# Performance work log

Hardware: AMD Instinct MI355X
Metric: run time of the kernel (lower is better)

The kernel has to match this reference:

```python
import jax, jax.numpy as jnp
import numpy as np

N_QUBITS = 10
DIM = 768
N_LAYERS = 3
BATCH = 2048


def setup_inputs() -> dict:
    key = jax.random.key(0)
    ks = jax.random.split(key, 5)
    z_i = jax.random.normal(ks[0], (BATCH, DIM), jnp.float32)
    W_in = jax.random.normal(ks[1], (DIM, N_QUBITS), jnp.float32) / np.sqrt(DIM).astype(np.float32)
    b_in = jnp.zeros((N_QUBITS,), jnp.float32)
    # torch.rand(shape) * pi  -> uniform [0, pi)
    weights = jax.random.uniform(ks[2], (N_LAYERS, N_QUBITS, 3), jnp.float32) * np.float32(np.pi)
    W_out = jax.random.normal(ks[3], (N_QUBITS, DIM), jnp.float32) / np.sqrt(N_QUBITS).astype(np.float32)
    b_out = jnp.zeros((DIM,), jnp.float32)
    return {"z_i": z_i, "W_in": W_in, "b_in": b_in, "weights": weights, "W_out": W_out, "b_out": b_out}


def _apply_gate(state, gate, q):
    """Apply a 1-qubit gate on wire q (wire 0 = most significant bit, PennyLane order).
    state: (B, 2**n) complex64; gate: (2,2) shared or (B,2,2) per-sample."""
    B, dim = state.shape
    left = 2 ** q
    right = dim // (2 * left)
    s = state.reshape(B, left, 2, right)
    eq = 'bij,bkjl->bkil' if gate.ndim == 3 else 'ij,bkjl->bkil'
    return jnp.einsum(eq, gate, s).reshape(B, dim)


def _apply_cnot(state, c, t, n):
    B = state.shape[0]
    s = state.reshape((B,) + (2,) * n)
    s = jnp.moveaxis(s, (1 + c, 1 + t), (1, 2))
    # control=1 block: flip target bit
    s = jnp.concatenate([s[:, :1], s[:, 1:, ::-1]], axis=1)
    s = jnp.moveaxis(s, (1, 2), (1 + c, 1 + t))
    return s.reshape(B, -1)


def _circuit(angles, weights):
    """AngleEmbedding (RX) + StronglyEntanglingLayers (Rot + ring of CNOTs), PauliZ expvals."""
    B, n = angles.shape
    L = weights.shape[0]
    state = jnp.zeros((B, 2 ** n), jnp.complex64).at[:, 0].set(1.0)
    # AngleEmbedding: RX(a) = [[cos(a/2), -i sin(a/2)], [-i sin(a/2), cos(a/2)]], per sample
    half = (0.5 * angles).astype(jnp.complex64)
    c = jnp.cos(half)
    s = -1j * jnp.sin(half)
    for q in range(n):
        g = jnp.stack([jnp.stack([c[:, q], s[:, q]], -1),
                       jnp.stack([s[:, q], c[:, q]], -1)], -2)  # (B,2,2)
        state = _apply_gate(state, g, q)
    wc = weights.astype(jnp.complex64)
    for l in range(L):
        for q in range(n):
            phi, theta, omega = wc[l, q, 0], wc[l, q, 1], wc[l, q, 2]
            ct = jnp.cos(0.5 * theta)
            st = jnp.sin(0.5 * theta)
            # Rot(phi,theta,omega) = RZ(omega) RY(theta) RZ(phi)
            g = jnp.stack([
                jnp.stack([jnp.exp(-0.5j * (phi + omega)) * ct, -jnp.exp(0.5j * (phi - omega)) * st]),
                jnp.stack([jnp.exp(-0.5j * (phi - omega)) * st, jnp.exp(0.5j * (phi + omega)) * ct]),
            ])
            state = _apply_gate(state, g, q)
        r = (l % (n - 1)) + 1  # PennyLane default ranges
        for i in range(n):
            state = _apply_cnot(state, i, (i + r) % n, n)
    probs = (state.real ** 2 + state.imag ** 2).reshape((B,) + (2,) * n)
    evs = []
    for w in range(n):
        axes = tuple(a for a in range(1, n + 1) if a != 1 + w)
        pw = probs.sum(axes)  # (B, 2)
        evs.append(pw[:, 0] - pw[:, 1])  # <Z_w>
    return jnp.stack(evs, -1)  # (B, n) float32


def reference(z_i, W_in, b_in, weights, W_out, b_out):
    # torch code detaches the projected angles before the qnode (.cpu().detach())
    angles = jax.lax.stop_gradient(z_i @ W_in + b_in)  # (B, n_qubits)
    evs = _circuit(angles, weights)
    return evs @ W_out + b_out  # (B, classical_input_dim)
```

## Files before the change

### kernel.cpp

```cpp
#include <hip/hip_runtime.h>

typedef float f2 __attribute__((ext_vector_type(2)));
typedef float f4 __attribute__((ext_vector_type(4)));

constexpr int NQ   = 10;
constexpr int CDIM = 768;
constexpr int NL   = 3;
constexpr int NREG = 16;
constexpr int WPB  = 4;


template<int CTRL>
__device__ __forceinline__ float dppmov(float x) {
    return __int_as_float(__builtin_amdgcn_update_dpp(
        __float_as_int(x), __float_as_int(x), CTRL, 0xF, 0xF, true));
}

template<int MASK>
__device__ __forceinline__ float lxor(float x, int lane) {
    static_assert(MASK == 1 || MASK == 2 || MASK == 4 || MASK == 8, "");
    if constexpr (MASK == 1)      return dppmov<0xB1>(x);
    else if constexpr (MASK == 2) return dppmov<0x4E>(x);
    else if constexpr (MASK == 4) {
        const float a = dppmov<0x104>(x);
        const float b = dppmov<0x114>(x);
        return ((lane >> 2) & 1) ? b : a;
    }
    else                          return dppmov<0x128>(x);
}

template<int B>
__device__ __forceinline__ void swap2(float x, float& lo, float& hi) {
    const unsigned xu = __float_as_uint(x);
#if __has_builtin(__builtin_amdgcn_permlane16_swap) && __has_builtin(__builtin_amdgcn_permlane32_swap)
    if constexpr (B == 4) {
        auto r = __builtin_amdgcn_permlane16_swap(xu, xu, false, false);
        lo = __uint_as_float(r[0]); hi = __uint_as_float(r[1]);
    } else {
        auto r = __builtin_amdgcn_permlane32_swap(xu, xu, false, false);
        lo = __uint_as_float(r[0]); hi = __uint_as_float(r[1]);
    }
#else
    float d, s;
    if constexpr (B == 4)
        asm("v_mov_b32 %0, %2\n\tv_mov_b32 %1, %2\n\ts_nop 1\n\t"
            "v_permlane16_swap_b32 %0, %1"
            : "=&v"(d), "=&v"(s) : "v"(x));
    else
        asm("v_mov_b32 %0, %2\n\tv_mov_b32 %1, %2\n\ts_nop 1\n\t"
            "v_permlane32_swap_b32 %0, %1"
            : "=&v"(d), "=&v"(s) : "v"(x));
    lo = d; hi = s;
#endif
}

__device__ __forceinline__ float wave_sum(float v) {
    v += dppmov<0xB1>(v);
    v += dppmov<0x4E>(v);
    v += dppmov<0x141>(v);
    v += dppmov<0x140>(v);
    float lo, hi;
    swap2<4>(v, lo, hi); v = lo + hi;
    swap2<5>(v, lo, hi); v = lo + hi;
    return v;
}


__device__ __forceinline__ f2 swapneg(f2 b) { f2 r; r.x = -b.y; r.y = b.x; return r; }
__device__ __forceinline__ f2 cmul(f2 a, f2 b) { return b * a.x + swapneg(b) * a.y; }
__device__ __forceinline__ f2 cfma(f2 a, f2 b, f2 acc) { return acc + b * a.x + swapneg(b) * a.y; }


template<int B>
__device__ __forceinline__ void gate_bit(f2 (&v)[NREG], int lane,
                                         f2 g00, f2 g01, f2 g10, f2 g11) {
    if constexpr (B >= 6) {
        constexpr int rb = B - 6;
#pragma unroll
        for (int p = 0; p < NREG / 2; ++p) {
            const int r0 = ((p >> rb) << (rb + 1)) | (p & ((1 << rb) - 1));
            const int r1 = r0 | (1 << rb);
            const f2 a0 = v[r0], a1 = v[r1];
            v[r0] = cfma(g01, a1, cmul(g00, a0));
            v[r1] = cfma(g11, a1, cmul(g10, a0));
        }
    } else if constexpr (B >= 4) {
        const bool hb = (lane >> B) & 1;
        const f2 A  = hb ? g10 : g00;
        const f2 Bc = hb ? g11 : g01;
#pragma unroll
        for (int r = 0; r < NREG; ++r) {
            float lx, hx, ly, hy;
            swap2<B>(v[r].x, lx, hx);
            swap2<B>(v[r].y, ly, hy);
            f2 lo; lo.x = lx; lo.y = ly;
            f2 hi; hi.x = hx; hi.y = hy;
            v[r] = cfma(Bc, hi, cmul(A, lo));
        }
    } else {
        const bool hb = (lane >> B) & 1;
        const f2 cO = hb ? g11 : g00;
        const f2 cP = hb ? g10 : g01;
#pragma unroll
        for (int r = 0; r < NREG; ++r) {
            f2 p;
            p.x = lxor<(1 << B)>(v[r].x, lane);
            p.y = lxor<(1 << B)>(v[r].y, lane);
            v[r] = cfma(cP, p, cmul(cO, v[r]));
        }
    }
}

template<int BT>
__device__ __forceinline__ float partner(float x, int lane) {
    if constexpr (BT >= 4) {
        float lo, hi; swap2<BT>(x, lo, hi);
        return ((lane >> BT) & 1) ? lo : hi;
    } else return lxor<(1 << BT)>(x, lane);
}


template<int BC, int BT>
__device__ __forceinline__ void cnot(f2 (&v)[NREG], int lane) {
    if constexpr (BC >= 6 && BT >= 6) {
        constexpr int rc = BC - 6, rt = BT - 6;
#pragma unroll
        for (int r = 0; r < NREG; ++r)
            if (((r >> rc) & 1) && !((r >> rt) & 1)) {
                const int r1 = r | (1 << rt);
                const f2 t = v[r]; v[r] = v[r1]; v[r1] = t;
            }
    } else if constexpr (BC >= 6) {
        constexpr int rc = BC - 6;
#pragma unroll
        for (int r = 0; r < NREG; ++r)
            if ((r >> rc) & 1) {
                f2 n;
                n.x = partner<BT>(v[r].x, lane);
                n.y = partner<BT>(v[r].y, lane);
                v[r] = n;
            }
    } else if constexpr (BT >= 6) {
        constexpr int rt = BT - 6;
        const bool c = (lane >> BC) & 1;
#pragma unroll
        for (int p = 0; p < NREG / 2; ++p) {
            const int r0 = ((p >> rt) << (rt + 1)) | (p & ((1 << rt) - 1));
            const int r1 = r0 | (1 << rt);
            const f2 a = v[r0], b = v[r1];
            v[r0] = c ? b : a;
            v[r1] = c ? a : b;
        }
    } else {
        const bool c = (lane >> BC) & 1;
#pragma unroll
        for (int r = 0; r < NREG; ++r) {
            f2 n;
            n.x = c ? partner<BT>(v[r].x, lane) : v[r].x;
            n.y = c ? partner<BT>(v[r].y, lane) : v[r].y;
            v[r] = n;
        }
    }
}


template<int Q = 0>
__device__ __forceinline__ void rot_layer_lds(f2 (&v)[NREG], int lane,
                                              const float4* g ) {
    if constexpr (Q < NQ) {
        const float4 p0 = g[Q * 2];
        const float4 p1 = g[Q * 2 + 1];
        f2 g00 = {p0.x, p0.y}, g01 = {p0.z, p0.w};
        f2 g10 = {p1.x, p1.y}, g11 = {p1.z, p1.w};
        gate_bit<9 - Q>(v, lane, g00, g01, g10, g11);
        rot_layer_lds<Q + 1>(v, lane, g);
    }
}

template<int L, int I = 0>
__device__ __forceinline__ void cnot_ring(f2 (&v)[NREG], int lane) {
    if constexpr (I < NQ) {
        constexpr int R = (L % (NQ - 1)) + 1;
        cnot<9 - I, 9 - ((I + R) % NQ)>(v, lane);
        cnot_ring<L, I + 1>(v, lane);
    }
}

constexpr unsigned ring2_mask(int w) {
    unsigned M[NQ] = {};
    for (int i = 0; i < NQ; ++i) M[i] = 1u << (9 - i);
    for (int i = 0; i < NQ; ++i) M[(i + 3) % NQ] ^= M[i];
    return M[w];
}

template<unsigned MR>
__device__ __forceinline__ float regsum16(const float (&pr)[NREG]) {
    float s = 0.f;
#pragma unroll
    for (int r = 0; r < NREG; ++r)
        s = (__builtin_popcount((unsigned)r & MR) & 1) ? s - pr[r] : s + pr[r];
    return s;
}

template<int W = 0>
__device__ __forceinline__ void measure_all(const float (&pr)[NREG], int lane,
                                            float (&ev)[NQ]) {
    if constexpr (W < NQ) {
        constexpr unsigned m  = ring2_mask(W);
        constexpr unsigned mr = (m >> 6) & 0xFu;
        constexpr unsigned ml = m & 63u;
        float s = regsum16<mr>(pr);
        if constexpr (ml != 0) {
            const unsigned flip = (unsigned)((__popc(lane & (int)ml) & 1)) << 31;
            s = __uint_as_float(__float_as_uint(s) ^ flip);
        }
        ev[W] = wave_sum(s);
        measure_all<W + 1>(pr, lane, ev);
    }
}

__global__ __launch_bounds__(64 * WPB, 2) void qembed(
    const float* __restrict__ z,
    const float* __restrict__ Win,
    const float* __restrict__ bin,
    const float* __restrict__ wts,
    const float* __restrict__ Wout,
    const float* __restrict__ bout,
    float* __restrict__ out)
{
    __shared__ float4 gl4[NL][NQ][2];

    const int wave = threadIdx.x >> 6;
    const int lane = threadIdx.x & 63;
    const int samp = blockIdx.x * WPB + wave;

    if (threadIdx.x < NL * NQ) {
        const int li = threadIdx.x / NQ, q = threadIdx.x % NQ;
        const float* wp = wts + (li * NQ + q) * 3;
        const float phi = wp[0], th = wp[1], om = wp[2];
        float st, ct, sA, cA, sB, cB;
        __sincosf(0.5f * th, &st, &ct);
        __sincosf(0.5f * (phi + om), &sA, &cA);
        __sincosf(0.5f * (phi - om), &sB, &cB);
        gl4[li][q][0] = make_float4( ct * cA, -ct * sA, -st * cB, -st * sB);
        gl4[li][q][1] = make_float4( st * cB, -st * sB,  ct * cA,  ct * sA);
    }

    float ang[NQ];
    {
        const float* zrow = z + (size_t)samp * CDIM;
        f2 a5[NQ / 2];
#pragma unroll
        for (int h = 0; h < NQ / 2; ++h) a5[h] = (f2){0.f, 0.f};
#pragma unroll
        for (int j = 0; j < 3; ++j) {
            const int kb = 4 * (lane + 64 * j);
            const float4 zv = *(const float4*)(zrow + kb);
            float w40[40];
#pragma unroll
            for (int t = 0; t < 10; ++t) {
                const float4 u = *(const float4*)(Win + (size_t)kb * NQ + 4 * t);
                w40[4 * t] = u.x; w40[4 * t + 1] = u.y;
                w40[4 * t + 2] = u.z; w40[4 * t + 3] = u.w;
            }
            const float zc[4] = {zv.x, zv.y, zv.z, zv.w};
#pragma unroll
            for (int c = 0; c < 4; ++c)
#pragma unroll
                for (int h = 0; h < NQ / 2; ++h) {
                    f2 w; w.x = w40[c * 10 + 2 * h]; w.y = w40[c * 10 + 2 * h + 1];
                    a5[h] += w * zc[c];
                }
        }
#pragma unroll
        for (int h = 0; h < NQ / 2; ++h) {
            ang[2 * h]     = wave_sum(a5[h].x) + bin[2 * h];
            ang[2 * h + 1] = wave_sum(a5[h].y) + bin[2 * h + 1];
        }
    }

    __syncthreads();

    f2 f0[NQ], f1[NQ];
#pragma unroll
    for (int q = 0; q < NQ; ++q) {
        const float4 p0 = gl4[0][q][0];
        const float4 p1 = gl4[0][q][1];
        float s, c;
        __sincosf(0.5f * ang[q], &s, &c);
        f2 a, b;
        a.x = p0.x * c + s * p0.w;  a.y = p0.y * c - s * p0.z;
        b.x = p1.x * c + s * p1.w;  b.y = p1.y * c - s * p1.z;
        f0[q] = a; f1[q] = b;
    }

    const int gray = lane ^ (lane >> 1);
    const int l0 = lane & 1;
    const int l5 = (lane >> 5) & 1;
    f2 G0 = ((gray >> 0) & 1) ? f1[9] : f0[9];
    f2 G1 = ((gray >> 1) & 1) ? f1[8] : f0[8];
    f2 G2 = ((gray >> 2) & 1) ? f1[7] : f0[7];
    f2 G3 = ((gray >> 3) & 1) ? f1[6] : f0[6];
    f2 G4 = ((gray >> 4) & 1) ? f1[5] : f0[5];
    const f2 L5 = cmul(cmul(G0, G1), cmul(G2, cmul(G3, G4)));
    f2 B5[2];
    B5[0] = l5 ? f1[4] : f0[4];
    B5[1] = l5 ? f0[4] : f1[4];
    f2 D8[2], E9[2];
    D8[0] = l0 ? f1[1] : f0[1];
    D8[1] = l0 ? f0[1] : f1[1];
    E9[0] = l0 ? f1[0] : f0[0];
    E9[1] = l0 ? f0[0] : f1[0];

    f2 P1[2];
    P1[0] = cmul(L5, B5[0]);
    P1[1] = cmul(L5, B5[1]);
    f2 P2[4];
#pragma unroll
    for (int r1b = 0; r1b < 2; ++r1b)
#pragma unroll
        for (int r0b = 0; r0b < 2; ++r0b)
            P2[r0b + 2 * r1b] = cmul(P1[r0b], (r0b ^ r1b) ? f1[3] : f0[3]);
    f2 P3[8];
#pragma unroll
    for (int r2b = 0; r2b < 2; ++r2b)
#pragma unroll
        for (int p = 0; p < 4; ++p)
            P3[p + 4 * r2b] = cmul(P2[p], (((p >> 1) & 1) ^ r2b) ? f1[2] : f0[2]);
    f2 W[4];
#pragma unroll
    for (int d = 0; d < 2; ++d)
#pragma unroll
        for (int u = 0; u < 2; ++u)
            W[u + 2 * d] = cmul(D8[u], E9[d]);

    f2 v[NREG];
#pragma unroll
    for (int r = 0; r < NREG; ++r) {
        const int r2b = (r >> 2) & 1, r3b = (r >> 3) & 1;
        v[r] = cmul(P3[r & 7], W[(r2b ^ r3b) + 2 * r3b]);
    }

#pragma unroll 1
    for (int l = 0; l < 2; ++l) {
        rot_layer_lds(v, lane, &gl4[l + 1][0][0]);
        if (l == 0) cnot_ring<1>(v, lane);
    }

    float pr[NREG];
#pragma unroll
    for (int r = 0; r < NREG; ++r) pr[r] = v[r].x * v[r].x + v[r].y * v[r].y;

    float ev[NQ];
    measure_all(pr, lane, ev);

#pragma unroll 1
    for (int ch = 0; ch < 3; ++ch) {
        const int d0 = ch * 256 + lane * 4;
        f4 w4[NQ];
#pragma unroll
        for (int q = 0; q < NQ; ++q) w4[q] = *(const f4*)(Wout + q * CDIM + d0);
        f4 o = *(const f4*)(bout + d0);
#pragma unroll
        for (int q = 0; q < NQ; ++q) o += w4[q] * ev[q];
        *(f4*)(out + (size_t)samp * CDIM + d0) = o;
    }
}

extern "C" void kernel_launch(void* const* d_in, const int* in_sizes, int n_in,
                              void* d_out, int out_size, void* d_ws, size_t ws_size,
                              hipStream_t stream) {
    const float* z    = (const float*)d_in[0];
    const float* Win  = (const float*)d_in[1];
    const float* bin  = (const float*)d_in[2];
    const float* wts  = (const float*)d_in[3];
    const float* Wout = (const float*)d_in[4];
    const float* bout = (const float*)d_in[5];
    float* outp       = (float*)d_out;

    const int batch  = in_sizes[0] / CDIM;
    const int blocks = batch / WPB;
    qembed<<<blocks, 64 * WPB, 0, stream>>>(z, Win, bin, wts, Wout, bout, outp);
}
```

Measured before the change: 27.18 us.

## Split each sample's statevector across two waves with LDS exchange for top qubit

Each sample now gets two wavefronts: each holds half the 1024-amplitude state (8 registers instead of 16), with the most significant qubit encoded by wave index. Gates and CNOTs that touch that qubit swap data through shared memory with block barriers, and expectation values are combined across the two waves through LDS. The output projection is also split between the waves. This halves the per-thread register footprint and doubles the wave count, which should raise occupancy and latency hiding. The cost is extra LDS traffic and several __syncthreads per layer.

After: 30.07 us. 1.11x slower.

```diff
diff --git a/kernel.cpp b/kernel.cpp
--- a/kernel.cpp
+++ b/kernel.cpp
@@ -1,13 +1,11 @@
 #include <hip/hip_runtime.h>
 
 typedef float f2 __attribute__((ext_vector_type(2)));
-typedef float f4 __attribute__((ext_vector_type(4)));
 
 constexpr int NQ   = 10;
 constexpr int CDIM = 768;
 constexpr int NL   = 3;
-constexpr int NREG = 16;
-constexpr int WPB  = 4;
+constexpr int NR   = 8;
 
 
 template<int CTRL>
@@ -44,12 +42,10 @@
     float d, s;
     if constexpr (B == 4)
         asm("v_mov_b32 %0, %2\n\tv_mov_b32 %1, %2\n\ts_nop 1\n\t"
-            "v_permlane16_swap_b32 %0, %1"
-            : "=&v"(d), "=&v"(s) : "v"(x));
+            "v_permlane16_swap_b32 %0, %1" : "=&v"(d), "=&v"(s) : "v"(x));
     else
         asm("v_mov_b32 %0, %2\n\tv_mov_b32 %1, %2\n\ts_nop 1\n\t"
-            "v_permlane32_swap_b32 %0, %1"
-            : "=&v"(d), "=&v"(s) : "v"(x));
+            "v_permlane32_swap_b32 %0, %1" : "=&v"(d), "=&v"(s) : "v"(x));
     lo = d; hi = s;
 #endif
 }
@@ -72,12 +68,13 @@
 
 
 template<int B>
-__device__ __forceinline__ void gate_bit(f2 (&v)[NREG], int lane,
+__device__ __forceinline__ void gate_bit(f2 (&v)[NR], int lane,
                                          f2 g00, f2 g01, f2 g10, f2 g11) {
+    static_assert(B <= 8, "");
     if constexpr (B >= 6) {
         constexpr int rb = B - 6;
 #pragma unroll
-        for (int p = 0; p < NREG / 2; ++p) {
+        for (int p = 0; p < NR / 2; ++p) {
             const int r0 = ((p >> rb) << (rb + 1)) | (p & ((1 << rb) - 1));
             const int r1 = r0 | (1 << rb);
             const f2 a0 = v[r0], a1 = v[r1];
@@ -89,7 +86,7 @@
         const f2 A  = hb ? g10 : g00;
         const f2 Bc = hb ? g11 : g01;
 #pragma unroll
-        for (int r = 0; r < NREG; ++r) {
+        for (int r = 0; r < NR; ++r) {
             float lx, hx, ly, hy;
             swap2<B>(v[r].x, lx, hx);
             swap2<B>(v[r].y, ly, hy);
@@ -102,7 +99,7 @@
         const f2 cO = hb ? g11 : g00;
         const f2 cP = hb ? g10 : g01;
 #pragma unroll
-        for (int r = 0; r < NREG; ++r) {
+        for (int r = 0; r < NR; ++r) {
             f2 p;
             p.x = lxor<(1 << B)>(v[r].x, lane);
             p.y = lxor<(1 << B)>(v[r].y, lane);
@@ -121,11 +118,44 @@
 
 
 template<int BC, int BT>
-__device__ __forceinline__ void cnot(f2 (&v)[NREG], int lane) {
-    if constexpr (BC >= 6 && BT >= 6) {
+__device__ __forceinline__ void cnot(f2 (&v)[NR], int lane, int hs,
+                                     f2* mybuf, const f2* pbuf) {
+    if constexpr (BC == 9) {
+        if (hs) {
+            if constexpr (BT >= 6) {
+                constexpr int rt = BT - 6;
+#pragma unroll
+                for (int p = 0; p < NR / 2; ++p) {
+                    const int r0 = ((p >> rt) << (rt + 1)) | (p & ((1 << rt) - 1));
+                    const int r1 = r0 | (1 << rt);
+                    const f2 t = v[r0]; v[r0] = v[r1]; v[r1] = t;
+                }
+            } else {
+#pragma unroll
+                for (int r = 0; r < NR; ++r) {
+                    f2 n;
+                    n.x = partner<BT>(v[r].x, lane);
+                    n.y = partner<BT>(v[r].y, lane);
+                    v[r] = n;
+                }
+            }
+        }
+    } else if constexpr (BT == 9) {
+        static_assert(BC < 6, "");
+#pragma unroll
+        for (int r = 0; r < NR; ++r) mybuf[r * 64 + lane] = v[r];
+        __syncthreads();
+        const bool c = (lane >> BC) & 1;
+#pragma unroll
+        for (int r = 0; r < NR; ++r) {
+            const f2 pv = pbuf[r * 64 + lane];
+            v[r] = c ? pv : v[r];
+        }
+        __syncthreads();
+    } else if constexpr (BC >= 6 && BT >= 6) {
         constexpr int rc = BC - 6, rt = BT - 6;
 #pragma unroll
-        for (int r = 0; r < NREG; ++r)
+        for (int r = 0; r < NR; ++r)
             if (((r >> rc) & 1) && !((r >> rt) & 1)) {
                 const int r1 = r | (1 << rt);
                 const f2 t = v[r]; v[r] = v[r1]; v[r1] = t;
@@ -133,7 +163,7 @@
     } else if constexpr (BC >= 6) {
         constexpr int rc = BC - 6;
 #pragma unroll
-        for (int r = 0; r < NREG; ++r)
+        for (int r = 0; r < NR; ++r)
             if ((r >> rc) & 1) {
                 f2 n;
                 n.x = partner<BT>(v[r].x, lane);
@@ -144,7 +174,7 @@
         constexpr int rt = BT - 6;
         const bool c = (lane >> BC) & 1;
 #pragma unroll
-        for (int p = 0; p < NREG / 2; ++p) {
+        for (int p = 0; p < NR / 2; ++p) {
             const int r0 = ((p >> rt) << (rt + 1)) | (p & ((1 << rt) - 1));
             const int r1 = r0 | (1 << rt);
             const f2 a = v[r0], b = v[r1];
@@ -154,7 +184,7 @@
     } else {
         const bool c = (lane >> BC) & 1;
 #pragma unroll
-        for (int r = 0; r < NREG; ++r) {
+        for (int r = 0; r < NR; ++r) {
             f2 n;
             n.x = c ? partner<BT>(v[r].x, lane) : v[r].x;
             n.y = c ? partner<BT>(v[r].y, lane) : v[r].y;
@@ -164,25 +194,45 @@
 }
 
 
-template<int Q = 0>
-__device__ __forceinline__ void rot_layer_lds(f2 (&v)[NREG], int lane,
-                                              const float4* g ) {
+__device__ __forceinline__ void rot_wave_gate(f2 (&v)[NR], int lane, int hs,
+                                              f2* mybuf, const f2* pbuf,
+                                              const float4* g) {
+    const float4 p0 = g[0];
+    const float4 p1 = g[1];
+    f2 g00 = {p0.x, p0.y}, g01 = {p0.z, p0.w};
+    f2 g10 = {p1.x, p1.y}, g11 = {p1.z, p1.w};
+    const f2 cO = hs ? g11 : g00;
+    const f2 cP = hs ? g10 : g01;
+#pragma unroll
+    for (int r = 0; r < NR; ++r) mybuf[r * 64 + lane] = v[r];
+    __syncthreads();
+#pragma unroll
+    for (int r = 0; r < NR; ++r) {
+        const f2 pv = pbuf[r * 64 + lane];
+        v[r] = cfma(cP, pv, cmul(cO, v[r]));
+    }
+    __syncthreads();
+}
+
+template<int Q = 1>
+__device__ __forceinline__ void rot_layer_rest(f2 (&v)[NR], int lane,
+                                               const float4* g ) {
     if constexpr (Q < NQ) {
         const float4 p0 = g[Q * 2];
         const float4 p1 = g[Q * 2 + 1];
         f2 g00 = {p0.x, p0.y}, g01 = {p0.z, p0.w};
         f2 g10 = {p1.x, p1.y}, g11 = {p1.z, p1.w};
         gate_bit<9 - Q>(v, lane, g00, g01, g10, g11);
-        rot_layer_lds<Q + 1>(v, lane, g);
-    }
-}
-
-template<int L, int I = 0>
-__device__ __forceinline__ void cnot_ring(f2 (&v)[NREG], int lane) {
+        rot_layer_rest<Q + 1>(v, lane, g);
+    }
+}
+
+template<int I = 0>
+__device__ __forceinline__ void cnot_ring1(f2 (&v)[NR], int lane, int hs,
+                                           f2* mybuf, const f2* pbuf) {
     if constexpr (I < NQ) {
-        constexpr int R = (L % (NQ - 1)) + 1;
-        cnot<9 - I, 9 - ((I + R) % NQ)>(v, lane);
-        cnot_ring<L, I + 1>(v, lane);
+        cnot<9 - I, 9 - ((I + 2) % NQ)>(v, lane, hs, mybuf, pbuf);
+        cnot_ring1<I + 1>(v, lane, hs, mybuf, pbuf);
     }
 }
 
@@ -194,32 +244,35 @@
 }
 
 template<unsigned MR>
-__device__ __forceinline__ float regsum16(const float (&pr)[NREG]) {
+__device__ __forceinline__ float regsum8(const float (&pr)[NR]) {
     float s = 0.f;
 #pragma unroll
-    for (int r = 0; r < NREG; ++r)
+    for (int r = 0; r < NR; ++r)
         s = (__builtin_popcount((unsigned)r & MR) & 1) ? s - pr[r] : s + pr[r];
     return s;
 }
 
 template<int W = 0>
-__device__ __forceinline__ void measure_all(const float (&pr)[NREG], int lane,
+__device__ __forceinline__ void measure_all(const float (&pr)[NR], int lane, int hs,
                                             float (&ev)[NQ]) {
     if constexpr (W < NQ) {
         constexpr unsigned m  = ring2_mask(W);
-        constexpr unsigned mr = (m >> 6) & 0xFu;
+        constexpr unsigned mr = (m >> 6) & 0x7u;
+        constexpr unsigned mw = (m >> 9) & 0x1u;
         constexpr unsigned ml = m & 63u;
-        float s = regsum16<mr>(pr);
-        if constexpr (ml != 0) {
-            const unsigned flip = (unsigned)((__popc(lane & (int)ml) & 1)) << 31;
-            s = __uint_as_float(__float_as_uint(s) ^ flip);
-        }
+        float s = regsum8<mr>(pr);
+        unsigned par = 0;
+        if constexpr (ml != 0) par = (unsigned)(__popc(lane & (int)ml) & 1);
+        if constexpr (mw != 0) par ^= (unsigned)hs;
+        if constexpr (ml != 0 || mw != 0)
+            s = __uint_as_float(__float_as_uint(s) ^ (par << 31));
         ev[W] = wave_sum(s);
-        measure_all<W + 1>(pr, lane, ev);
-    }
-}
-
-__global__ __launch_bounds__(64 * WPB, 2) void qembed(
+        measure_all<W + 1>(pr, lane, hs, ev);
+    }
+}
+
+
+__global__ __launch_bounds__(128, 4) void qembed(
     const float* __restrict__ z,
     const float* __restrict__ Win,
     const float* __restrict__ bin,
@@ -229,10 +282,15 @@
     float* __restrict__ out)
 {
     __shared__ float4 gl4[NL][NQ][2];
+    __shared__ f2 xch[2][NR * 64];
+    __shared__ float sev[2][NQ];
 
     const int wave = threadIdx.x >> 6;
     const int lane = threadIdx.x & 63;
-    const int samp = blockIdx.x * WPB + wave;
+    const int hs   = wave;
+    const int samp = blockIdx.x;
+    f2* mybuf      = xch[wave];
+    const f2* pbuf = xch[wave ^ 1];
 
     if (threadIdx.x < NL * NQ) {
         const int li = threadIdx.x / NQ, q = threadIdx.x % NQ;
@@ -295,22 +353,21 @@
     }
 
     const int gray = lane ^ (lane >> 1);
-    const int l0 = lane & 1;
-    const int l5 = (lane >> 5) & 1;
+    const int l5  = (lane >> 5) & 1;
+    const int l0h = (lane & 1) ^ hs;
     f2 G0 = ((gray >> 0) & 1) ? f1[9] : f0[9];
     f2 G1 = ((gray >> 1) & 1) ? f1[8] : f0[8];
     f2 G2 = ((gray >> 2) & 1) ? f1[7] : f0[7];
     f2 G3 = ((gray >> 3) & 1) ? f1[6] : f0[6];
     f2 G4 = ((gray >> 4) & 1) ? f1[5] : f0[5];
-    const f2 L5 = cmul(cmul(G0, G1), cmul(G2, cmul(G3, G4)));
+    f2 L5 = cmul(cmul(G0, G1), cmul(G2, cmul(G3, G4)));
+    L5 = cmul(L5, l0h ? f1[0] : f0[0]);
     f2 B5[2];
     B5[0] = l5 ? f1[4] : f0[4];
     B5[1] = l5 ? f0[4] : f1[4];
-    f2 D8[2], E9[2];
-    D8[0] = l0 ? f1[1] : f0[1];
-    D8[1] = l0 ? f0[1] : f1[1];
-    E9[0] = l0 ? f1[0] : f0[0];
-    E9[1] = l0 ? f0[0] : f1[0];
+    f2 D8[2];
+    D8[0] = l0h ? f1[1] : f0[1];
+    D8[1] = l0h ? f0[1] : f1[1];
 
     f2 P1[2];
     P1[0] = cmul(L5, B5[0]);
@@ -327,43 +384,43 @@
 #pragma unroll
         for (int p = 0; p < 4; ++p)
             P3[p + 4 * r2b] = cmul(P2[p], (((p >> 1) & 1) ^ r2b) ? f1[2] : f0[2]);
-    f2 W[4];
-#pragma unroll
-    for (int d = 0; d < 2; ++d)
-#pragma unroll
-        for (int u = 0; u < 2; ++u)
-            W[u + 2 * d] = cmul(D8[u], E9[d]);
-
-    f2 v[NREG];
-#pragma unroll
-    for (int r = 0; r < NREG; ++r) {
-        const int r2b = (r >> 2) & 1, r3b = (r >> 3) & 1;
-        v[r] = cmul(P3[r & 7], W[(r2b ^ r3b) + 2 * r3b]);
-    }
+
+    f2 v[NR];
+#pragma unroll
+    for (int r = 0; r < NR; ++r) v[r] = cmul(P3[r], D8[(r >> 2) & 1]);
 
 #pragma unroll 1
     for (int l = 0; l < 2; ++l) {
-        rot_layer_lds(v, lane, &gl4[l + 1][0][0]);
-        if (l == 0) cnot_ring<1>(v, lane);
-    }
-
-    float pr[NREG];
-#pragma unroll
-    for (int r = 0; r < NREG; ++r) pr[r] = v[r].x * v[r].x + v[r].y * v[r].y;
+        rot_wave_gate(v, lane, hs, mybuf, pbuf, &gl4[l + 1][0][0]);
+        rot_layer_rest(v, lane, &gl4[l + 1][0][0]);
+        if (l == 0) cnot_ring1(v, lane, hs, mybuf, pbuf);
+    }
+
+    float pr[NR];
+#pragma unroll
+    for (int r = 0; r < NR; ++r) pr[r] = v[r].x * v[r].x + v[r].y * v[r].y;
 
     float ev[NQ];
-    measure_all(pr, lane, ev);
+    measure_all(pr, lane, hs, ev);
+
+    if (lane == 0) {
+#pragma unroll
+        for (int w = 0; w < NQ; ++w) sev[wave][w] = ev[w];
+    }
+    __syncthreads();
+#pragma unroll
+    for (int w = 0; w < NQ; ++w) ev[w] += sev[wave ^ 1][w];
 
 #pragma unroll 1
-    for (int ch = 0; ch < 3; ++ch) {
-        const int d0 = ch * 256 + lane * 4;
-        f4 w4[NQ];
-#pragma unroll
-        for (int q = 0; q < NQ; ++q) w4[q] = *(const f4*)(Wout + q * CDIM + d0);
-        f4 o = *(const f4*)(bout + d0);
-#pragma unroll
-        for (int q = 0; q < NQ; ++q) o += w4[q] * ev[q];
-        *(f4*)(out + (size_t)samp * CDIM + d0) = o;
+    for (int it = 0; it < 3; ++it) {
+        const int d0 = hs * 384 + it * 128 + lane * 2;
+        f2 w2[NQ];
+#pragma unroll
+        for (int q = 0; q < NQ; ++q) w2[q] = *(const f2*)(Wout + q * CDIM + d0);
+        f2 o = *(const f2*)(bout + d0);
+#pragma unroll
+        for (int q = 0; q < NQ; ++q) o += w2[q] * ev[q];
+        *(f2*)(out + (size_t)samp * CDIM + d0) = o;
     }
 }
 
@@ -378,7 +435,6 @@
     const float* bout = (const float*)d_in[5];
     float* outp       = (float*)d_out;
 
-    const int batch  = in_sizes[0] / CDIM;
-    const int blocks = batch / WPB;
-    qembed<<<blocks, 64 * WPB, 0, stream>>>(z, Win, bin, wts, Wout, bout, outp);
-}
+    const int batch = in_sizes[0] / CDIM;
+    qembed<<<batch, 128, 0, stream>>>(z, Win, bin, wts, Wout, bout, outp);
+}
```

## Process two samples per wave with packed f2 state vectors

Applied to the files above, without the earlier changes.

Each wave now simulates two samples at once, storing real and imaginary parts as f2 pairs so packed FP32 math and each DPP/permlane shuffle serve both samples. The input projection, measurement reductions and output projection also handle both samples, sharing the W_in and W_out loads. The grid is halved and launch bounds drop to one block per SIMD-occupancy hint, trading parallelism and occupancy for per-wave throughput, with higher register pressure.

After: 24.23 us. 10.8% less time.

```diff
diff --git a/kernel.cpp b/kernel.cpp
--- a/kernel.cpp
+++ b/kernel.cpp
@@ -27,6 +27,14 @@
         return ((lane >> 2) & 1) ? b : a;
     }
     else                          return dppmov<0x128>(x);
+}
+
+template<int MASK>
+__device__ __forceinline__ f2 lxor2(f2 x, int lane) {
+    f2 r;
+    r.x = lxor<MASK>(x.x, lane);
+    r.y = lxor<MASK>(x.y, lane);
+    return r;
 }
 
 template<int B>
@@ -44,14 +52,21 @@
     float d, s;
     if constexpr (B == 4)
         asm("v_mov_b32 %0, %2\n\tv_mov_b32 %1, %2\n\ts_nop 1\n\t"
-            "v_permlane16_swap_b32 %0, %1"
-            : "=&v"(d), "=&v"(s) : "v"(x));
+            "v_permlane16_swap_b32 %0, %1" : "=&v"(d), "=&v"(s) : "v"(x));
     else
         asm("v_mov_b32 %0, %2\n\tv_mov_b32 %1, %2\n\ts_nop 1\n\t"
-            "v_permlane32_swap_b32 %0, %1"
-            : "=&v"(d), "=&v"(s) : "v"(x));
+            "v_permlane32_swap_b32 %0, %1" : "=&v"(d), "=&v"(s) : "v"(x));
     lo = d; hi = s;
 #endif
+}
+
+template<int B>
+__device__ __forceinline__ void swap2v(f2 x, f2& lo, f2& hi) {
+    float lx, hx, ly, hy;
+    swap2<B>(x.x, lx, hx);
+    swap2<B>(x.y, ly, hy);
+    lo.x = lx; lo.y = ly;
+    hi.x = hx; hi.y = hy;
 }
 
 __device__ __forceinline__ float wave_sum(float v) {
@@ -65,14 +80,34 @@
     return v;
 }
 
+__device__ __forceinline__ f2 wave_sum2(f2 v) {
+    f2 r;
+    r.x = wave_sum(v.x);
+    r.y = wave_sum(v.y);
+    return r;
+}
+
+
+struct c2 { f2 re, im; };
+
+__device__ __forceinline__ c2 cmulP(f2 g, c2 a) {
+    c2 r;
+    r.re = a.re * g.x - a.im * g.y;
+    r.im = a.im * g.x + a.re * g.y;
+    return r;
+}
+__device__ __forceinline__ c2 cfmaP(f2 g, c2 a, c2 acc) {
+    acc.re += a.re * g.x - a.im * g.y;
+    acc.im += a.im * g.x + a.re * g.y;
+    return acc;
+}
 
 __device__ __forceinline__ f2 swapneg(f2 b) { f2 r; r.x = -b.y; r.y = b.x; return r; }
 __device__ __forceinline__ f2 cmul(f2 a, f2 b) { return b * a.x + swapneg(b) * a.y; }
-__device__ __forceinline__ f2 cfma(f2 a, f2 b, f2 acc) { return acc + b * a.x + swapneg(b) * a.y; }
 
 
 template<int B>
-__device__ __forceinline__ void gate_bit(f2 (&v)[NREG], int lane,
+__device__ __forceinline__ void gate_bit(c2 (&v)[NREG], int lane,
                                          f2 g00, f2 g01, f2 g10, f2 g11) {
     if constexpr (B >= 6) {
         constexpr int rb = B - 6;
@@ -80,9 +115,9 @@
         for (int p = 0; p < NREG / 2; ++p) {
             const int r0 = ((p >> rb) << (rb + 1)) | (p & ((1 << rb) - 1));
             const int r1 = r0 | (1 << rb);
-            const f2 a0 = v[r0], a1 = v[r1];
-            v[r0] = cfma(g01, a1, cmul(g00, a0));
-            v[r1] = cfma(g11, a1, cmul(g10, a0));
+            const c2 a0 = v[r0], a1 = v[r1];
+            v[r0] = cfmaP(g01, a1, cmulP(g00, a0));
+            v[r1] = cfmaP(g11, a1, cmulP(g10, a0));
         }
     } else if constexpr (B >= 4) {
         const bool hb = (lane >> B) & 1;
@@ -90,12 +125,10 @@
         const f2 Bc = hb ? g11 : g01;
 #pragma unroll
         for (int r = 0; r < NREG; ++r) {
-            float lx, hx, ly, hy;
-            swap2<B>(v[r].x, lx, hx);
-            swap2<B>(v[r].y, ly, hy);
-            f2 lo; lo.x = lx; lo.y = ly;
-            f2 hi; hi.x = hx; hi.y = hy;
-            v[r] = cfma(Bc, hi, cmul(A, lo));
+            c2 lo, hi;
+            swap2v<B>(v[r].re, lo.re, hi.re);
+            swap2v<B>(v[r].im, lo.im, hi.im);
+            v[r] = cfmaP(Bc, hi, cmulP(A, lo));
         }
     } else {
         const bool hb = (lane >> B) & 1;
@@ -103,41 +136,45 @@
         const f2 cP = hb ? g10 : g01;
 #pragma unroll
         for (int r = 0; r < NREG; ++r) {
-            f2 p;
-            p.x = lxor<(1 << B)>(v[r].x, lane);
-            p.y = lxor<(1 << B)>(v[r].y, lane);
-            v[r] = cfma(cP, p, cmul(cO, v[r]));
+            c2 p;
+            p.re = lxor2<(1 << B)>(v[r].re, lane);
+            p.im = lxor2<(1 << B)>(v[r].im, lane);
+            v[r] = cfmaP(cP, p, cmulP(cO, v[r]));
         }
     }
 }
 
 template<int BT>
-__device__ __forceinline__ float partner(float x, int lane) {
+__device__ __forceinline__ f2 partner2(f2 x, int lane) {
     if constexpr (BT >= 4) {
-        float lo, hi; swap2<BT>(x, lo, hi);
-        return ((lane >> BT) & 1) ? lo : hi;
-    } else return lxor<(1 << BT)>(x, lane);
+        f2 lo, hi;
+        swap2v<BT>(x, lo, hi);
+        f2 r;
+        r.x = ((lane >> BT) & 1) ? lo.x : hi.x;
+        r.y = ((lane >> BT) & 1) ? lo.y : hi.y;
+        return r;
+    } else return lxor2<(1 << BT)>(x, lane);
 }
 
 
 template<int BC, int BT>
-__device__ __forceinline__ void cnot(f2 (&v)[NREG], int lane) {
+__device__ __forceinline__ void cnot(c2 (&v)[NREG], int lane) {
     if constexpr (BC >= 6 && BT >= 6) {
         constexpr int rc = BC - 6, rt = BT - 6;
 #pragma unroll
         for (int r = 0; r < NREG; ++r)
             if (((r >> rc) & 1) && !((r >> rt) & 1)) {
                 const int r1 = r | (1 << rt);
-                const f2 t = v[r]; v[r] = v[r1]; v[r1] = t;
+                const c2 t = v[r]; v[r] = v[r1]; v[r1] = t;
             }
     } else if constexpr (BC >= 6) {
         constexpr int rc = BC - 6;
 #pragma unroll
         for (int r = 0; r < NREG; ++r)
             if ((r >> rc) & 1) {
-                f2 n;
-                n.x = partner<BT>(v[r].x, lane);
-                n.y = partner<BT>(v[r].y, lane);
+                c2 n;
+                n.re = partner2<BT>(v[r].re, lane);
+                n.im = partner2<BT>(v[r].im, lane);
                 v[r] = n;
             }
     } else if constexpr (BT >= 6) {
@@ -147,25 +184,25 @@
         for (int p = 0; p < NREG / 2; ++p) {
             const int r0 = ((p >> rt) << (rt + 1)) | (p & ((1 << rt) - 1));
             const int r1 = r0 | (1 << rt);
-            const f2 a = v[r0], b = v[r1];
-            v[r0] = c ? b : a;
-            v[r1] = c ? a : b;
+            const c2 a = v[r0], b = v[r1];
+            v[r0].re = c ? b.re : a.re;  v[r0].im = c ? b.im : a.im;
+            v[r1].re = c ? a.re : b.re;  v[r1].im = c ? a.im : b.im;
         }
     } else {
         const bool c = (lane >> BC) & 1;
 #pragma unroll
         for (int r = 0; r < NREG; ++r) {
-            f2 n;
-            n.x = c ? partner<BT>(v[r].x, lane) : v[r].x;
-            n.y = c ? partner<BT>(v[r].y, lane) : v[r].y;
-            v[r] = n;
+            const f2 pre = partner2<BT>(v[r].re, lane);
+            const f2 pim = partner2<BT>(v[r].im, lane);
+            v[r].re = c ? pre : v[r].re;
+            v[r].im = c ? pim : v[r].im;
         }
     }
 }
 
 
 template<int Q = 0>
-__device__ __forceinline__ void rot_layer_lds(f2 (&v)[NREG], int lane,
+__device__ __forceinline__ void rot_layer_lds(c2 (&v)[NREG], int lane,
                                               const float4* g ) {
     if constexpr (Q < NQ) {
         const float4 p0 = g[Q * 2];
@@ -178,7 +215,7 @@
 }
 
 template<int L, int I = 0>
-__device__ __forceinline__ void cnot_ring(f2 (&v)[NREG], int lane) {
+__device__ __forceinline__ void cnot_ring(c2 (&v)[NREG], int lane) {
     if constexpr (I < NQ) {
         constexpr int R = (L % (NQ - 1)) + 1;
         cnot<9 - I, 9 - ((I + R) % NQ)>(v, lane);
@@ -194,8 +231,8 @@
 }
 
 template<unsigned MR>
-__device__ __forceinline__ float regsum16(const float (&pr)[NREG]) {
-    float s = 0.f;
+__device__ __forceinline__ f2 regsum16(const f2 (&pr)[NREG]) {
+    f2 s = {0.f, 0.f};
 #pragma unroll
     for (int r = 0; r < NREG; ++r)
         s = (__builtin_popcount((unsigned)r & MR) & 1) ? s - pr[r] : s + pr[r];
@@ -203,23 +240,24 @@
 }
 
 template<int W = 0>
-__device__ __forceinline__ void measure_all(const float (&pr)[NREG], int lane,
-                                            float (&ev)[NQ]) {
+__device__ __forceinline__ void measure_all(const f2 (&pr)[NREG], int lane,
+                                            f2 (&ev)[NQ]) {
     if constexpr (W < NQ) {
         constexpr unsigned m  = ring2_mask(W);
         constexpr unsigned mr = (m >> 6) & 0xFu;
         constexpr unsigned ml = m & 63u;
-        float s = regsum16<mr>(pr);
+        f2 s = regsum16<mr>(pr);
         if constexpr (ml != 0) {
             const unsigned flip = (unsigned)((__popc(lane & (int)ml) & 1)) << 31;
-            s = __uint_as_float(__float_as_uint(s) ^ flip);
-        }
-        ev[W] = wave_sum(s);
+            s.x = __uint_as_float(__float_as_uint(s.x) ^ flip);
+            s.y = __uint_as_float(__float_as_uint(s.y) ^ flip);
+        }
+        ev[W] = wave_sum2(s);
         measure_all<W + 1>(pr, lane, ev);
     }
 }
 
-__global__ __launch_bounds__(64 * WPB, 2) void qembed(
+__global__ __launch_bounds__(64 * WPB, 1) void qembed(
     const float* __restrict__ z,
     const float* __restrict__ Win,
     const float* __restrict__ bin,
@@ -230,9 +268,9 @@
 {
     __shared__ float4 gl4[NL][NQ][2];
 
-    const int wave = threadIdx.x >> 6;
-    const int lane = threadIdx.x & 63;
-    const int samp = blockIdx.x * WPB + wave;
+    const int wave  = threadIdx.x >> 6;
+    const int lane  = threadIdx.x & 63;
+    const int samp0 = (blockIdx.x * WPB + wave) * 2;
 
     if (threadIdx.x < NL * NQ) {
         const int li = threadIdx.x / NQ, q = threadIdx.x % NQ;
@@ -246,16 +284,18 @@
         gl4[li][q][1] = make_float4( st * cB, -st * sB,  ct * cA,  ct * sA);
     }
 
-    float ang[NQ];
+    f2 ang[NQ];
     {
-        const float* zrow = z + (size_t)samp * CDIM;
-        f2 a5[NQ / 2];
-#pragma unroll
-        for (int h = 0; h < NQ / 2; ++h) a5[h] = (f2){0.f, 0.f};
+        const float* z0 = z + (size_t)samp0 * CDIM;
+        const float* z1 = z0 + CDIM;
+        f2 acc[NQ];
+#pragma unroll
+        for (int q = 0; q < NQ; ++q) acc[q] = (f2){0.f, 0.f};
 #pragma unroll
         for (int j = 0; j < 3; ++j) {
             const int kb = 4 * (lane + 64 * j);
-            const float4 zv = *(const float4*)(zrow + kb);
+            const float4 za = *(const float4*)(z0 + kb);
+            const float4 zb = *(const float4*)(z1 + kb);
             float w40[40];
 #pragma unroll
             for (int t = 0; t < 10; ++t) {
@@ -263,82 +303,84 @@
                 w40[4 * t] = u.x; w40[4 * t + 1] = u.y;
                 w40[4 * t + 2] = u.z; w40[4 * t + 3] = u.w;
             }
-            const float zc[4] = {zv.x, zv.y, zv.z, zv.w};
-#pragma unroll
-            for (int c = 0; c < 4; ++c)
-#pragma unroll
-                for (int h = 0; h < NQ / 2; ++h) {
-                    f2 w; w.x = w40[c * 10 + 2 * h]; w.y = w40[c * 10 + 2 * h + 1];
-                    a5[h] += w * zc[c];
-                }
-        }
-#pragma unroll
-        for (int h = 0; h < NQ / 2; ++h) {
-            ang[2 * h]     = wave_sum(a5[h].x) + bin[2 * h];
-            ang[2 * h + 1] = wave_sum(a5[h].y) + bin[2 * h + 1];
-        }
+            const float za4[4] = {za.x, za.y, za.z, za.w};
+            const float zb4[4] = {zb.x, zb.y, zb.z, zb.w};
+#pragma unroll
+            for (int c = 0; c < 4; ++c) {
+                f2 zp; zp.x = za4[c]; zp.y = zb4[c];
+#pragma unroll
+                for (int q = 0; q < NQ; ++q) acc[q] += zp * w40[c * 10 + q];
+            }
+        }
+#pragma unroll
+        for (int q = 0; q < NQ; ++q) ang[q] = wave_sum2(acc[q]) + bin[q];
     }
 
     __syncthreads();
 
-    f2 f0[NQ], f1[NQ];
-#pragma unroll
-    for (int q = 0; q < NQ; ++q) {
-        const float4 p0 = gl4[0][q][0];
-        const float4 p1 = gl4[0][q][1];
-        float s, c;
-        __sincosf(0.5f * ang[q], &s, &c);
-        f2 a, b;
-        a.x = p0.x * c + s * p0.w;  a.y = p0.y * c - s * p0.z;
-        b.x = p1.x * c + s * p1.w;  b.y = p1.y * c - s * p1.z;
-        f0[q] = a; f1[q] = b;
-    }
-
-    const int gray = lane ^ (lane >> 1);
-    const int l0 = lane & 1;
-    const int l5 = (lane >> 5) & 1;
-    f2 G0 = ((gray >> 0) & 1) ? f1[9] : f0[9];
-    f2 G1 = ((gray >> 1) & 1) ? f1[8] : f0[8];
-    f2 G2 = ((gray >> 2) & 1) ? f1[7] : f0[7];
-    f2 G3 = ((gray >> 3) & 1) ? f1[6] : f0[6];
-    f2 G4 = ((gray >> 4) & 1) ? f1[5] : f0[5];
-    const f2 L5 = cmul(cmul(G0, G1), cmul(G2, cmul(G3, G4)));
-    f2 B5[2];
-    B5[0] = l5 ? f1[4] : f0[4];
-    B5[1] = l5 ? f0[4] : f1[4];
-    f2 D8[2], E9[2];
-    D8[0] = l0 ? f1[1] : f0[1];
-    D8[1] = l0 ? f0[1] : f1[1];
-    E9[0] = l0 ? f1[0] : f0[0];
-    E9[1] = l0 ? f0[0] : f1[0];
-
-    f2 P1[2];
-    P1[0] = cmul(L5, B5[0]);
-    P1[1] = cmul(L5, B5[1]);
-    f2 P2[4];
-#pragma unroll
-    for (int r1b = 0; r1b < 2; ++r1b)
-#pragma unroll
-        for (int r0b = 0; r0b < 2; ++r0b)
-            P2[r0b + 2 * r1b] = cmul(P1[r0b], (r0b ^ r1b) ? f1[3] : f0[3]);
-    f2 P3[8];
-#pragma unroll
-    for (int r2b = 0; r2b < 2; ++r2b)
-#pragma unroll
-        for (int p = 0; p < 4; ++p)
-            P3[p + 4 * r2b] = cmul(P2[p], (((p >> 1) & 1) ^ r2b) ? f1[2] : f0[2]);
-    f2 W[4];
-#pragma unroll
-    for (int d = 0; d < 2; ++d)
-#pragma unroll
-        for (int u = 0; u < 2; ++u)
-            W[u + 2 * d] = cmul(D8[u], E9[d]);
-
-    f2 v[NREG];
-#pragma unroll
-    for (int r = 0; r < NREG; ++r) {
-        const int r2b = (r >> 2) & 1, r3b = (r >> 3) & 1;
-        v[r] = cmul(P3[r & 7], W[(r2b ^ r3b) + 2 * r3b]);
+    c2 v[NREG];
+#pragma unroll
+    for (int s = 0; s < 2; ++s) {
+        f2 f0[NQ], f1[NQ];
+#pragma unroll
+        for (int q = 0; q < NQ; ++q) {
+            const float4 p0 = gl4[0][q][0];
+            const float4 p1 = gl4[0][q][1];
+            const float aq = s ? ang[q].y : ang[q].x;
+            float sn, cs;
+            __sincosf(0.5f * aq, &sn, &cs);
+            f2 a, b;
+            a.x = p0.x * cs + sn * p0.w;  a.y = p0.y * cs - sn * p0.z;
+            b.x = p1.x * cs + sn * p1.w;  b.y = p1.y * cs - sn * p1.z;
+            f0[q] = a; f1[q] = b;
+        }
+        const int gray = lane ^ (lane >> 1);
+        const int l0 = lane & 1;
+        const int l5 = (lane >> 5) & 1;
+        f2 G0 = ((gray >> 0) & 1) ? f1[9] : f0[9];
+        f2 G1 = ((gray >> 1) & 1) ? f1[8] : f0[8];
+        f2 G2 = ((gray >> 2) & 1) ? f1[7] : f0[7];
+        f2 G3 = ((gray >> 3) & 1) ? f1[6] : f0[6];
+        f2 G4 = ((gray >> 4) & 1) ? f1[5] : f0[5];
+        const f2 L5 = cmul(cmul(G0, G1), cmul(G2, cmul(G3, G4)));
+        f2 B5[2];
+        B5[0] = l5 ? f1[4] : f0[4];
+        B5[1] = l5 ? f0[4] : f1[4];
+        f2 D8[2], E9[2];
+        D8[0] = l0 ? f1[1] : f0[1];
+        D8[1] = l0 ? f0[1] : f1[1];
+        E9[0] = l0 ? f1[0] : f0[0];
+        E9[1] = l0 ? f0[0] : f1[0];
+
+        f2 P1[2];
+        P1[0] = cmul(L5, B5[0]);
+        P1[1] = cmul(L5, B5[1]);
+        f2 P2[4];
+#pragma unroll
+        for (int r1b = 0; r1b < 2; ++r1b)
+#pragma unroll
+            for (int r0b = 0; r0b < 2; ++r0b)
+                P2[r0b + 2 * r1b] = cmul(P1[r0b], (r0b ^ r1b) ? f1[3] : f0[3]);
+        f2 P3[8];
+#pragma unroll
+        for (int r2b = 0; r2b < 2; ++r2b)
+#pragma unroll
+            for (int p = 0; p < 4; ++p)
+                P3[p + 4 * r2b] = cmul(P2[p], (((p >> 1) & 1) ^ r2b) ? f1[2] : f0[2]);
+        f2 W[4];
+#pragma unroll
+        for (int d = 0; d < 2; ++d)
+#pragma unroll
+            for (int u = 0; u < 2; ++u)
+                W[u + 2 * d] = cmul(D8[u], E9[d]);
+
+#pragma unroll
+        for (int r = 0; r < NREG; ++r) {
+            const int r2b = (r >> 2) & 1, r3b = (r >> 3) & 1;
+            const f2 amp = cmul(P3[r & 7], W[(r2b ^ r3b) + 2 * r3b]);
+            if (s == 0) { v[r].re.x = amp.x; v[r].im.x = amp.y; }
+            else        { v[r].re.y = amp.x; v[r].im.y = amp.y; }
+        }
     }
 
 #pragma unroll 1
@@ -347,11 +389,12 @@
         if (l == 0) cnot_ring<1>(v, lane);
     }
 
-    float pr[NREG];
-#pragma unroll
-    for (int r = 0; r < NREG; ++r) pr[r] = v[r].x * v[r].x + v[r].y * v[r].y;
-
-    float ev[NQ];
+    f2 pr[NREG];
+#pragma unroll
+    for (int r = 0; r < NREG; ++r)
+        pr[r] = v[r].re * v[r].re + v[r].im * v[r].im;
+
+    f2 ev[NQ];
     measure_all(pr, lane, ev);
 
 #pragma unroll 1
@@ -360,10 +403,15 @@
         f4 w4[NQ];
 #pragma unroll
         for (int q = 0; q < NQ; ++q) w4[q] = *(const f4*)(Wout + q * CDIM + d0);
-        f4 o = *(const f4*)(bout + d0);
-#pragma unroll
-        for (int q = 0; q < NQ; ++q) o += w4[q] * ev[q];
-        *(f4*)(out + (size_t)samp * CDIM + d0) = o;
+        const f4 bo = *(const f4*)(bout + d0);
+        f4 o0 = bo, o1 = bo;
+#pragma unroll
+        for (int q = 0; q < NQ; ++q) {
+            o0 += w4[q] * ev[q].x;
+            o1 += w4[q] * ev[q].y;
+        }
+        *(f4*)(out + (size_t)samp0 * CDIM + d0) = o0;
+        *(f4*)(out + (size_t)(samp0 + 1) * CDIM + d0) = o1;
     }
 }
 
@@ -379,6 +427,6 @@
     float* outp       = (float*)d_out;
 
     const int batch  = in_sizes[0] / CDIM;
-    const int blocks = batch / WPB;
+    const int blocks = batch / (2 * WPB);
     qembed<<<blocks, 64 * WPB, 0, stream>>>(z, Win, bin, wts, Wout, bout, outp);
 }
```
